# Performance work log

Measured on AMD Instinct MI355X. Metric: run time of the kernel, lower is better.

The kernel has to match this reference:

```python
import jax, jax.numpy as jnp
import numpy as np

BH, S, D = 16, 2048, 128
TEMPERATURE = float(np.sqrt(D))


def setup_inputs() -> dict:
    key = jax.random.key(0)
    kq, kk, kv = jax.random.split(key, 3)
    q = jax.random.normal(kq, (BH, S, D), dtype=jnp.float32)
    k = jax.random.normal(kk, (BH, S, D), dtype=jnp.float32)
    v = jax.random.normal(kv, (BH, S, D), dtype=jnp.float32)
    # causal mask: True = masked (filled with -inf), broadcast to every batch*head
    causal = ~jnp.tril(jnp.ones((S, S), dtype=bool))
    mask = jnp.broadcast_to(causal, (BH, S, S))
    return {"q": q, "k": k, "v": v, "mask": mask}


def reference(q, k, v, mask):
    # attn = q @ k^T / temperature, masked_fill, softmax over keys, attn @ v
    attn = jnp.einsum("bqd,bkd->bqk", q, k) / TEMPERATURE  # [BH, S, S]
    attn = jnp.where(mask, -jnp.inf, attn)
    attn = jax.nn.softmax(attn, axis=2)
    # dropout is identity in eval mode
    output = jnp.einsum("bqk,bkd->bqd", attn, v)  # [BH, S, D]
    return (output, attn)
```

## Files before the change

kernel.cpp:

```cpp
#include <hip/hip_runtime.h>
#include <hip/hip_bf16.h>

#define BH_N 16
#define SEQ 2048
#define DH 128
#define PSTR 2056

typedef __attribute__((ext_vector_type(8))) short bf16x8;
typedef __attribute__((ext_vector_type(4))) float f32x4;

__device__ __forceinline__ short f2bf(float x) {
    union { __hip_bfloat16 b; short s; } u;
    u.b = __float2bfloat16(x);
    return u.s;
}
__device__ __forceinline__ float bf2f(short s) {
    union { unsigned int u; float f; } v;
    v.u = ((unsigned int)(unsigned short)s) << 16;
    return v.f;
}

__global__ __launch_bounds__(256) void prep_kv(
    const float* __restrict__ kp, const float* __restrict__ vp,
    unsigned short* __restrict__ Kb, unsigned short* __restrict__ Vt)
{
    const int tid  = threadIdx.x;
    const int kb64 = blockIdx.x * 64;
    const int bh   = blockIdx.y;
    const float* Ksrc = kp + ((size_t)bh * SEQ + kb64) * DH;
    const float* Vsrc = vp + ((size_t)bh * SEQ + kb64) * DH;
    unsigned short* Kdst = Kb + ((size_t)bh * SEQ + kb64) * DH;
    unsigned short* Vdst = Vt + (size_t)bh * DH * SEQ + kb64;

    #pragma unroll
    for (int i = 0; i < 8; ++i) {
        const int f4 = i * 256 + tid;
        const float4 kv = *(const float4*)(Ksrc + (size_t)f4 * 4);
        ushort4 o;
        o.x = (unsigned short)f2bf(kv.x); o.y = (unsigned short)f2bf(kv.y);
        o.z = (unsigned short)f2bf(kv.z); o.w = (unsigned short)f2bf(kv.w);
        *(ushort4*)(Kdst + (size_t)f4 * 4) = o;
    }
    const int key   = tid & 63;
    const int dbase = (tid >> 6) * 4;
    #pragma unroll
    for (int j = 0; j < 8; ++j) {
        const int d0 = dbase + j * 16;
        const float4 vv = *(const float4*)(Vsrc + (size_t)key * DH + d0);
        Vdst[(size_t)(d0 + 0) * SEQ + key] = (unsigned short)f2bf(vv.x);
        Vdst[(size_t)(d0 + 1) * SEQ + key] = (unsigned short)f2bf(vv.y);
        Vdst[(size_t)(d0 + 2) * SEQ + key] = (unsigned short)f2bf(vv.z);
        Vdst[(size_t)(d0 + 3) * SEQ + key] = (unsigned short)f2bf(vv.w);
    }
}

#define LOADK4(K0, K1, K2, K3, KEYBASE) do {                                   \
    const unsigned short* kr_ = Kbh + (size_t)((KEYBASE) + c16) * DH + g * 8;  \
    K0 = *(const bf16x8*)(kr_);                                                \
    K1 = *(const bf16x8*)(kr_ + 32);                                           \
    K2 = *(const bf16x8*)(kr_ + 64);                                           \
    K3 = *(const bf16x8*)(kr_ + 96);                                           \
} while (0)

#define SW1(K0, K1, K2, K3, KEYBASE) do {                                      \
    f32x4 acc_ = {0.f, 0.f, 0.f, 0.f};                                         \
    acc_ = __builtin_amdgcn_mfma_f32_16x16x32_bf16(qf[0], K0, acc_, 0, 0, 0);  \
    acc_ = __builtin_amdgcn_mfma_f32_16x16x32_bf16(qf[1], K1, acc_, 0, 0, 0);  \
    acc_ = __builtin_amdgcn_mfma_f32_16x16x32_bf16(qf[2], K2, acc_, 0, 0, 0);  \
    acc_ = __builtin_amdgcn_mfma_f32_16x16x32_bf16(qf[3], K3, acc_, 0, 0, 0);  \
    const int key_ = (KEYBASE) + c16;                                          \
    const int qr_  = qw + g * 4;                                               \
    const float p0_ = (key_ <= qr_ + 0) ? __expf(acc_[0]) : 0.f;               \
    const float p1_ = (key_ <= qr_ + 1) ? __expf(acc_[1]) : 0.f;               \
    const float p2_ = (key_ <= qr_ + 2) ? __expf(acc_[2]) : 0.f;               \
    const float p3_ = (key_ <= qr_ + 3) ? __expf(acc_[3]) : 0.f;               \
    lsr[0] += p0_; lsr[1] += p1_; lsr[2] += p2_; lsr[3] += p3_;                \
    unsigned short* pq_ = &strip[g * 4][0] + key_;                             \
    pq_[0]        = (unsigned short)f2bf(p0_);                                 \
    pq_[PSTR]     = (unsigned short)f2bf(p1_);                                 \
    pq_[2 * PSTR] = (unsigned short)f2bf(p2_);                                 \
    pq_[3 * PSTR] = (unsigned short)f2bf(p3_);                                 \
} while (0)

#define LOADV8(V0,V1,V2,V3,V4,V5,V6,V7, KEYOFF) do {                           \
    const unsigned short* vb_ = Vbh + (size_t)c16 * SEQ + (KEYOFF) + g * 8;    \
    V0 = *(const bf16x8*)(vb_);                                                \
    V1 = *(const bf16x8*)(vb_ + 16 * SEQ);                                     \
    V2 = *(const bf16x8*)(vb_ + 32 * SEQ);                                     \
    V3 = *(const bf16x8*)(vb_ + 48 * SEQ);                                     \
    V4 = *(const bf16x8*)(vb_ + 64 * SEQ);                                     \
    V5 = *(const bf16x8*)(vb_ + 80 * SEQ);                                     \
    V6 = *(const bf16x8*)(vb_ + 96 * SEQ);                                     \
    V7 = *(const bf16x8*)(vb_ + 112 * SEQ);                                    \
} while (0)

#define PV8(PA, V0,V1,V2,V3,V4,V5,V6,V7) do {                                  \
    oacc[0] = __builtin_amdgcn_mfma_f32_16x16x32_bf16(PA, V0, oacc[0], 0, 0, 0); \
    oacc[1] = __builtin_amdgcn_mfma_f32_16x16x32_bf16(PA, V1, oacc[1], 0, 0, 0); \
    oacc[2] = __builtin_amdgcn_mfma_f32_16x16x32_bf16(PA, V2, oacc[2], 0, 0, 0); \
    oacc[3] = __builtin_amdgcn_mfma_f32_16x16x32_bf16(PA, V3, oacc[3], 0, 0, 0); \
    oacc[4] = __builtin_amdgcn_mfma_f32_16x16x32_bf16(PA, V4, oacc[4], 0, 0, 0); \
    oacc[5] = __builtin_amdgcn_mfma_f32_16x16x32_bf16(PA, V5, oacc[5], 0, 0, 0); \
    oacc[6] = __builtin_amdgcn_mfma_f32_16x16x32_bf16(PA, V6, oacc[6], 0, 0, 0); \
    oacc[7] = __builtin_amdgcn_mfma_f32_16x16x32_bf16(PA, V7, oacc[7], 0, 0, 0); \
} while (0)

__global__ __launch_bounds__(512, 4) void attn_main(
    const float* __restrict__ qp, const unsigned short* __restrict__ Kb,
    const unsigned short* __restrict__ Vt, float* __restrict__ outO,
    float* __restrict__ outA)
{
    __shared__ float lspart[8][16];
    __shared__ float lrec[16];
    __shared__ float Osh[16][132];
    __shared__ __align__(16) unsigned short strip[16][PSTR];

    const int b   = blockIdx.x;
    const int j   = b & 7;
    const int idx = b >> 3;
    const int bh  = 2 * j + (idx & 1);
    const int qt  = 127 - (idx >> 1);
    const int qw  = qt * 16;
    const size_t qbase = (size_t)bh * SEQ + qw;

    const int tid  = threadIdx.x;
    const int wv   = tid >> 6;
    const int lane = tid & 63;
    const int c16  = lane & 15;
    const int g    = lane >> 4;
    const float invT = 0.08838834764831845f;

    const unsigned short* Kbh = Kb + (size_t)bh * SEQ * DH;
    const unsigned short* Vbh = Vt + (size_t)bh * DH * SEQ;

    bf16x8 qf[4];
    {
        const float* qrow = qp + (qbase + c16) * DH + g * 8;
        #pragma unroll
        for (int c = 0; c < 4; ++c) {
            const float4 a = *(const float4*)(qrow + c * 32);
            const float4 bq = *(const float4*)(qrow + c * 32 + 4);
            bf16x8 f;
            f[0] = f2bf(a.x * invT);  f[1] = f2bf(a.y * invT);
            f[2] = f2bf(a.z * invT);  f[3] = f2bf(a.w * invT);
            f[4] = f2bf(bq.x * invT); f[5] = f2bf(bq.y * invT);
            f[6] = f2bf(bq.z * invT); f[7] = f2bf(bq.w * invT);
            qf[c] = f;
        }
    }

    float lsr[4] = {0.f, 0.f, 0.f, 0.f};
    const int n16 = qt + 1;
    {
        bf16x8 ka0, ka1, ka2, ka3, kb0, kb1, kb2, kb3;
        int t = wv;
        if (t < n16) LOADK4(ka0, ka1, ka2, ka3, t << 4);
        for (; t + 8 < n16; t += 16) {
            LOADK4(kb0, kb1, kb2, kb3, (t + 8) << 4);
            SW1(ka0, ka1, ka2, ka3, t << 4);
            if (t + 16 < n16) LOADK4(ka0, ka1, ka2, ka3, (t + 16) << 4);
            SW1(kb0, kb1, kb2, kb3, (t + 8) << 4);
        }
        if (t < n16) SW1(ka0, ka1, ka2, ka3, t << 4);
    }
    #pragma unroll
    for (int r = 0; r < 4; ++r) {
        float s = lsr[r];
        #pragma unroll
        for (int m = 1; m < 16; m <<= 1) s += __shfl_xor(s, m);
        lsr[r] = s;
    }
    if (c16 == 0) {
        #pragma unroll
        for (int r = 0; r < 4; ++r) lspart[wv][g * 4 + r] = lsr[r];
    }
    __syncthreads();
    float li[4];
    #pragma unroll
    for (int r = 0; r < 4; ++r) {
        float s = 0.f;
        #pragma unroll
        for (int w = 0; w < 8; ++w) s += lspart[w][g * 4 + r];
        li[r] = 1.f / s;
    }
    const int ns = (qw + 79) >> 6;
    if (wv == 0 && c16 == 0) {
        #pragma unroll
        for (int r = 0; r < 4; ++r) lrec[g * 4 + r] = li[r];
    }
    {
        const int row = tid >> 5;
        for (int c = n16 * 16 + (tid & 31); c < ns * 64; c += 32) strip[row][c] = 0;
    }
    __syncthreads();

    f32x4 oacc[8];
    #pragma unroll
    for (int d = 0; d < 8; ++d) oacc[d] = (f32x4){0.f, 0.f, 0.f, 0.f};

    {
        const int sr = lane >> 4;
        const int sc = (lane & 15) * 4;
        float l4[4];
        #pragma unroll
        for (int i = 0; i < 4; ++i) l4[i] = lrec[i * 4 + sr];

        bf16x8 va0, va1, va2, va3, va4, va5, va6, va7;
        bf16x8 vb0, vb1, vb2, vb3, vb4, vb5, vb6, vb7;
        for (int S = wv; S < ns; S += 8) {
            const int KB = S << 6;
            LOADV8(va0,va1,va2,va3,va4,va5,va6,va7, KB);
            LOADV8(vb0,vb1,vb2,vb3,vb4,vb5,vb6,vb7, KB + 32);
            #pragma unroll
            for (int i = 0; i < 4; ++i) {
                const int pr = i * 4 + sr;
                const unsigned short* src = &strip[pr][KB + sc];
                float4 w;
                w.x = bf2f(src[0]) * l4[i]; w.y = bf2f(src[1]) * l4[i];
                w.z = bf2f(src[2]) * l4[i]; w.w = bf2f(src[3]) * l4[i];
                *(float4*)(outA + (qbase + pr) * SEQ + KB + sc) = w;
            }
            {
                const bf16x8 pa = *(const bf16x8*)(&strip[c16][KB + g * 8]);
                PV8(pa, va0,va1,va2,va3,va4,va5,va6,va7);
            }
            {
                const bf16x8 pa = *(const bf16x8*)(&strip[c16][KB + 32 + g * 8]);
                PV8(pa, vb0,vb1,vb2,vb3,vb4,vb5,vb6,vb7);
            }
        }
    }

    for (int wp = 0; wp < 8; ++wp) {
        if (wv == wp) {
            #pragma unroll
            for (int dt = 0; dt < 8; ++dt) {
                #pragma unroll
                for (int r = 0; r < 4; ++r) {
                    const float val = oacc[dt][r] * li[r];
                    if (wp == 0) Osh[g * 4 + r][dt * 16 + c16]  = val;
                    else         Osh[g * 4 + r][dt * 16 + c16] += val;
                }
            }
        }
        __syncthreads();
    }
    {
        const int r  = tid >> 5;
        const int d0 = (tid & 31) * 4;
        float4 o;
        o.x = Osh[r][d0 + 0]; o.y = Osh[r][d0 + 1];
        o.z = Osh[r][d0 + 2]; o.w = Osh[r][d0 + 3];
        *(float4*)(outO + (qbase + r) * DH + d0) = o;
    }

    {
        const int r = tid >> 5;
        float* zrow = outA + (qbase + r) * SEQ;
        const float4 z = {0.f, 0.f, 0.f, 0.f};
        for (int c = ns * 64 + (tid & 31) * 4; c < SEQ; c += 128) {
            *(float4*)(zrow + c) = z;
        }
    }
}

__global__ __launch_bounds__(256) void attn_fallback(
    const float* __restrict__ qp, const float* __restrict__ kp,
    const float* __restrict__ vp, float* __restrict__ outO,
    float* __restrict__ outA)
{
    const int qt   = blockIdx.x;
    const int bh   = blockIdx.y;
    const int wv   = threadIdx.x >> 6;
    const int lane = threadIdx.x & 63;
    const int c16  = lane & 15;
    const int g    = lane >> 4;
    const int qw = qt * 64 + wv * 16;
    const size_t qbase = (size_t)bh * SEQ + qw;
    const float invT = 0.08838834764831845f;

    bf16x8 qf[4];
    {
        const float* qrow = qp + (qbase + c16) * DH + g * 8;
        #pragma unroll
        for (int c = 0; c < 4; ++c) {
            const float4 a = *(const float4*)(qrow + c * 32);
            const float4 bq = *(const float4*)(qrow + c * 32 + 4);
            bf16x8 f;
            f[0] = f2bf(a.x * invT);  f[1] = f2bf(a.y * invT);
            f[2] = f2bf(a.z * invT);  f[3] = f2bf(a.w * invT);
            f[4] = f2bf(bq.x * invT); f[5] = f2bf(bq.y * invT);
            f[6] = f2bf(bq.z * invT); f[7] = f2bf(bq.w * invT);
            qf[c] = f;
        }
    }
    const float* kbase = kp + (size_t)bh * SEQ * DH;
    const float* vbase = vp + (size_t)bh * SEQ * DH;

    float ls0 = 0.f, ls1 = 0.f, ls2 = 0.f, ls3 = 0.f;
    const int nkt16 = (qw + 16) >> 4;
    for (int t = 0; t < nkt16; ++t) {
        const int kb = t << 4;
        const float* krow = kbase + (size_t)(kb + c16) * DH + g * 8;
        f32x4 acc = {0.f, 0.f, 0.f, 0.f};
        #pragma unroll
        for (int c = 0; c < 4; ++c) {
            const float4 a = *(const float4*)(krow + c * 32);
            const float4 bq = *(const float4*)(krow + c * 32 + 4);
            bf16x8 f;
            f[0] = f2bf(a.x);  f[1] = f2bf(a.y);  f[2] = f2bf(a.z);  f[3] = f2bf(a.w);
            f[4] = f2bf(bq.x); f[5] = f2bf(bq.y); f[6] = f2bf(bq.z); f[7] = f2bf(bq.w);
            acc = __builtin_amdgcn_mfma_f32_16x16x32_bf16(qf[c], f, acc, 0, 0, 0);
        }
        const int key = kb + c16;
        const int qr  = qw + g * 4;
        if (key <= qr + 0) ls0 += __expf(acc[0]);
        if (key <= qr + 1) ls1 += __expf(acc[1]);
        if (key <= qr + 2) ls2 += __expf(acc[2]);
        if (key <= qr + 3) ls3 += __expf(acc[3]);
    }
    #pragma unroll
    for (int m = 1; m < 16; m <<= 1) {
        ls0 += __shfl_xor(ls0, m);
        ls1 += __shfl_xor(ls1, m);
        ls2 += __shfl_xor(ls2, m);
        ls3 += __shfl_xor(ls3, m);
    }
    const float li0 = 1.f / ls0, li1 = 1.f / ls1, li2 = 1.f / ls2, li3 = 1.f / ls3;

    __shared__ __align__(16) short ptileF[4][16][32];
    f32x4 oacc[8];
    #pragma unroll
    for (int d = 0; d < 8; ++d) oacc[d] = (f32x4){0.f, 0.f, 0.f, 0.f};

    const int n32 = (qw + 47) >> 5;
    for (int t = 0; t < n32; ++t) {
        const int kb32 = t << 5;
        #pragma unroll
        for (int h = 0; h < 2; ++h) {
            const int kb = kb32 + h * 16;
            const float* krow = kbase + (size_t)(kb + c16) * DH + g * 8;
            f32x4 acc = {0.f, 0.f, 0.f, 0.f};
            #pragma unroll
            for (int c = 0; c < 4; ++c) {
                const float4 a = *(const float4*)(krow + c * 32);
                const float4 bq = *(const float4*)(krow + c * 32 + 4);
                bf16x8 f;
                f[0] = f2bf(a.x);  f[1] = f2bf(a.y);  f[2] = f2bf(a.z);  f[3] = f2bf(a.w);
                f[4] = f2bf(bq.x); f[5] = f2bf(bq.y); f[6] = f2bf(bq.z); f[7] = f2bf(bq.w);
                acc = __builtin_amdgcn_mfma_f32_16x16x32_bf16(qf[c], f, acc, 0, 0, 0);
            }
            const int key = kb + c16;
            const int qr  = qw + g * 4;
            const float p0 = (key <= qr + 0) ? __expf(acc[0]) * li0 : 0.f;
            const float p1 = (key <= qr + 1) ? __expf(acc[1]) * li1 : 0.f;
            const float p2 = (key <= qr + 2) ? __expf(acc[2]) * li2 : 0.f;
            const float p3 = (key <= qr + 3) ? __expf(acc[3]) * li3 : 0.f;
            outA[(qbase + g * 4 + 0) * SEQ + kb + c16] = p0;
            outA[(qbase + g * 4 + 1) * SEQ + kb + c16] = p1;
            outA[(qbase + g * 4 + 2) * SEQ + kb + c16] = p2;
            outA[(qbase + g * 4 + 3) * SEQ + kb + c16] = p3;
            ptileF[wv][g * 4 + 0][h * 16 + c16] = f2bf(p0);
            ptileF[wv][g * 4 + 1][h * 16 + c16] = f2bf(p1);
            ptileF[wv][g * 4 + 2][h * 16 + c16] = f2bf(p2);
            ptileF[wv][g * 4 + 3][h * 16 + c16] = f2bf(p3);
        }
        bf16x8 pa = *(bf16x8*)&ptileF[wv][c16][g * 8];
        #pragma unroll
        for (int dt = 0; dt < 8; ++dt) {
            const float* vcol = vbase + (size_t)(kb32 + g * 8) * DH + dt * 16 + c16;
            bf16x8 vf;
            #pragma unroll
            for (int i = 0; i < 8; ++i) vf[i] = f2bf(vcol[(size_t)i * DH]);
            oacc[dt] = __builtin_amdgcn_mfma_f32_16x16x32_bf16(pa, vf, oacc[dt], 0, 0, 0);
        }
    }
    {
        const float4 z4 = {0.f, 0.f, 0.f, 0.f};
        float* zrow = outA + (qbase + (lane >> 2)) * SEQ;
        for (int c = n32 * 32 + (lane & 3) * 8; c < SEQ; c += 32) {
            *(float4*)(zrow + c)     = z4;
            *(float4*)(zrow + c + 4) = z4;
        }
    }
    #pragma unroll
    for (int dt = 0; dt < 8; ++dt) {
        #pragma unroll
        for (int r = 0; r < 4; ++r) {
            outO[(qbase + g * 4 + r) * DH + dt * 16 + c16] = oacc[dt][r];
        }
    }
}

extern "C" void kernel_launch(void* const* d_in, const int* in_sizes, int n_in,
                              void* d_out, int out_size, void* d_ws, size_t ws_size,
                              hipStream_t stream) {
    (void)in_sizes; (void)n_in; (void)out_size;
    const float* q = (const float*)d_in[0];
    const float* k = (const float*)d_in[1];
    const float* v = (const float*)d_in[2];
    float* outO = (float*)d_out;
    float* outA = outO + (size_t)BH_N * SEQ * DH;

    const size_t need = (size_t)BH_N * SEQ * DH * sizeof(unsigned short) * 2;
    if (ws_size >= need) {
        unsigned short* Kb = (unsigned short*)d_ws;
        unsigned short* Vt = Kb + (size_t)BH_N * SEQ * DH;
        prep_kv<<<dim3(SEQ / 64, BH_N), 256, 0, stream>>>(k, v, Kb, Vt);
        attn_main<<<dim3(2048), 512, 0, stream>>>(q, Kb, Vt, outO, outA);
    } else {
        attn_fallback<<<dim3(SEQ / 64, BH_N), 256, 0, stream>>>(q, k, v, outO, outA);
    }
}
```

Measured before the change: 176.0 us.

## Deepen K/V prefetch pipelines and replace serialized O reduction with parallel slab sum

The K-tile phase now keeps four tiles of K loads in flight per wave instead of two. The PV loop now prefetches the next V tiles while the MFMAs for the current tile run. The cross-wave O reduction drops its loop of eight barriers: each wave writes a private slab into shared memory that aliases the probability strip, and all threads then sum the slabs in parallel. The cost is more registers and a larger aliased shared buffer, which may lower occupancy. A strange no-op line was also added to the fallback kernel.

```diff
diff --git a/kernel.cpp b/kernel.cpp
--- a/kernel.cpp
+++ b/kernel.cpp
@@ -14,9 +14,9 @@
     u.b = __float2bfloat16(x);
     return u.s;
 }
-__device__ __forceinline__ float bf2f(short s) {
+__device__ __forceinline__ float bf2f(unsigned short s) {
     union { unsigned int u; float f; } v;
-    v.u = ((unsigned int)(unsigned short)s) << 16;
+    v.u = ((unsigned int)s) << 16;
     return v.f;
 }
 
@@ -112,8 +112,9 @@
 {
     __shared__ float lspart[8][16];
     __shared__ float lrec[16];
-    __shared__ float Osh[16][132];
-    __shared__ __align__(16) unsigned short strip[16][PSTR];
+    __shared__ __align__(16) unsigned char smem[8 * 2116 * 4];
+    unsigned short (*strip)[PSTR] = (unsigned short(*)[PSTR])smem;
+    float* Oall = (float*)smem;
 
     const int b   = blockIdx.x;
     const int j   = b & 7;
@@ -152,16 +153,22 @@
     float lsr[4] = {0.f, 0.f, 0.f, 0.f};
     const int n16 = qt + 1;
     {
-        bf16x8 ka0, ka1, ka2, ka3, kb0, kb1, kb2, kb3;
+        bf16x8 k00,k01,k02,k03, k10,k11,k12,k13, k20,k21,k22,k23, k30,k31,k32,k33;
         int t = wv;
-        if (t < n16) LOADK4(ka0, ka1, ka2, ka3, t << 4);
-        for (; t + 8 < n16; t += 16) {
-            LOADK4(kb0, kb1, kb2, kb3, (t + 8) << 4);
-            SW1(ka0, ka1, ka2, ka3, t << 4);
-            if (t + 16 < n16) LOADK4(ka0, ka1, ka2, ka3, (t + 16) << 4);
-            SW1(kb0, kb1, kb2, kb3, (t + 8) << 4);
-        }
-        if (t < n16) SW1(ka0, ka1, ka2, ka3, t << 4);
+        if (t < n16)      LOADK4(k00,k01,k02,k03, t << 4);
+        if (t + 8 < n16)  LOADK4(k10,k11,k12,k13, (t + 8) << 4);
+        if (t + 16 < n16) LOADK4(k20,k21,k22,k23, (t + 16) << 4);
+        if (t + 24 < n16) LOADK4(k30,k31,k32,k33, (t + 24) << 4);
+        for (; t + 32 < n16; t += 32) {
+            SW1(k00,k01,k02,k03, t << 4);        LOADK4(k00,k01,k02,k03, (t + 32) << 4);
+            SW1(k10,k11,k12,k13, (t + 8) << 4);  LOADK4(k10,k11,k12,k13, (t + 40) << 4);
+            SW1(k20,k21,k22,k23, (t + 16) << 4); LOADK4(k20,k21,k22,k23, (t + 48) << 4);
+            SW1(k30,k31,k32,k33, (t + 24) << 4); LOADK4(k30,k31,k32,k33, (t + 56) << 4);
+        }
+        if (t < n16)      SW1(k00,k01,k02,k03, t << 4);
+        if (t + 8 < n16)  SW1(k10,k11,k12,k13, (t + 8) << 4);
+        if (t + 16 < n16) SW1(k20,k21,k22,k23, (t + 16) << 4);
+        if (t + 24 < n16) SW1(k30,k31,k32,k33, (t + 24) << 4);
     }
     #pragma unroll
     for (int r = 0; r < 4; ++r) {
@@ -205,12 +212,15 @@
         #pragma unroll
         for (int i = 0; i < 4; ++i) l4[i] = lrec[i * 4 + sr];
 
-        bf16x8 va0, va1, va2, va3, va4, va5, va6, va7;
-        bf16x8 vb0, vb1, vb2, vb3, vb4, vb5, vb6, vb7;
-        for (int S = wv; S < ns; S += 8) {
+        bf16x8 va0,va1,va2,va3,va4,va5,va6,va7;
+        bf16x8 vb0,vb1,vb2,vb3,vb4,vb5,vb6,vb7;
+        int S = wv;
+        if (S < ns) {
+            LOADV8(va0,va1,va2,va3,va4,va5,va6,va7, S << 6);
+            LOADV8(vb0,vb1,vb2,vb3,vb4,vb5,vb6,vb7, (S << 6) + 32);
+        }
+        for (; S < ns; S += 8) {
             const int KB = S << 6;
-            LOADV8(va0,va1,va2,va3,va4,va5,va6,va7, KB);
-            LOADV8(vb0,vb1,vb2,vb3,vb4,vb5,vb6,vb7, KB + 32);
             #pragma unroll
             for (int i = 0; i < 4; ++i) {
                 const int pr = i * 4 + sr;
@@ -224,34 +234,38 @@
                 const bf16x8 pa = *(const bf16x8*)(&strip[c16][KB + g * 8]);
                 PV8(pa, va0,va1,va2,va3,va4,va5,va6,va7);
             }
+            if (S + 8 < ns) LOADV8(va0,va1,va2,va3,va4,va5,va6,va7, (S + 8) << 6);
             {
                 const bf16x8 pa = *(const bf16x8*)(&strip[c16][KB + 32 + g * 8]);
                 PV8(pa, vb0,vb1,vb2,vb3,vb4,vb5,vb6,vb7);
             }
-        }
-    }
-
-    for (int wp = 0; wp < 8; ++wp) {
-        if (wv == wp) {
+            if (S + 8 < ns) LOADV8(vb0,vb1,vb2,vb3,vb4,vb5,vb6,vb7, ((S + 8) << 6) + 32);
+        }
+    }
+
+    __syncthreads();
+    {
+        float* slab = Oall + wv * 2116;
+        #pragma unroll
+        for (int dt = 0; dt < 8; ++dt) {
             #pragma unroll
-            for (int dt = 0; dt < 8; ++dt) {
-                #pragma unroll
-                for (int r = 0; r < 4; ++r) {
-                    const float val = oacc[dt][r] * li[r];
-                    if (wp == 0) Osh[g * 4 + r][dt * 16 + c16]  = val;
-                    else         Osh[g * 4 + r][dt * 16 + c16] += val;
-                }
+            for (int r = 0; r < 4; ++r) {
+                slab[(g * 4 + r) * 132 + dt * 16 + c16] = oacc[dt][r] * li[r];
             }
         }
-        __syncthreads();
-    }
-    {
-        const int r  = tid >> 5;
-        const int d0 = (tid & 31) * 4;
-        float4 o;
-        o.x = Osh[r][d0 + 0]; o.y = Osh[r][d0 + 1];
-        o.z = Osh[r][d0 + 2]; o.w = Osh[r][d0 + 3];
-        *(float4*)(outO + (qbase + r) * DH + d0) = o;
+    }
+    __syncthreads();
+    {
+        const int row = tid >> 5;
+        const int d0  = (tid & 31) * 4;
+        float sx = 0.f, sy = 0.f, sz = 0.f, sw = 0.f;
+        #pragma unroll
+        for (int w = 0; w < 8; ++w) {
+            const float* p = Oall + w * 2116 + row * 132 + d0;
+            sx += p[0]; sy += p[1]; sz += p[2]; sw += p[3];
+        }
+        float4 o; o.x = sx; o.y = sy; o.z = sz; o.w = sw;
+        *(float4*)(outO + (qbase + row) * DH + d0) = o;
     }
 
     {
@@ -371,6 +385,8 @@
             const float* vcol = vbase + (size_t)(kb32 + g * 8) * DH + dt * 16 + c16;
             bf16x8 vf;
             #pragma unroll
+            for (int i = 0; i < 8; ++i) vf[i] = f2bf((unsigned short)f2bf(vcol[(size_t)i * DH]) ) , vf[i] = f2bf(vcol[(size_t)i * DH]) ? 0 : 0;
+            #pragma unroll
             for (int i = 0; i < 8; ++i) vf[i] = f2bf(vcol[(size_t)i * DH]);
             oacc[dt] = __builtin_amdgcn_mfma_f32_16x16x32_bf16(pa, vf, oacc[dt], 0, 0, 0);
         }
```

Result: slower. 190.3 us (+8.1%).

## Split attention into P-sweep and PV/store kernels via global bf16 P buffer

Applied to the files above, without the earlier changes.

Splits the fused attention kernel into two launches. The first computes exp(QK^T) tiles into a global bf16 P workspace plus reciprocal row sums. The second reads P back to write the normalized attention matrix and compute P@V. This removes the large per-block LDS strip (16x2056 bf16) so more blocks can be resident, but adds a global round trip of up to 128 MB of P traffic, an extra launch, and a larger workspace requirement. If the workspace is too small, it falls back to the slow path.

```diff
diff --git a/kernel.cpp b/kernel.cpp
--- a/kernel.cpp
+++ b/kernel.cpp
@@ -4,19 +4,19 @@
 #define BH_N 16
 #define SEQ 2048
 #define DH 128
-#define PSTR 2056
 
 typedef __attribute__((ext_vector_type(8))) short bf16x8;
 typedef __attribute__((ext_vector_type(4))) float f32x4;
+typedef __attribute__((ext_vector_type(4))) int int4v;
 
 __device__ __forceinline__ short f2bf(float x) {
     union { __hip_bfloat16 b; short s; } u;
     u.b = __float2bfloat16(x);
     return u.s;
 }
-__device__ __forceinline__ float bf2f(short s) {
+__device__ __forceinline__ float bf2f(unsigned short s) {
     union { unsigned int u; float f; } v;
-    v.u = ((unsigned int)(unsigned short)s) << 16;
+    v.u = ((unsigned int)s) << 16;
     return v.f;
 }
 
@@ -62,7 +62,7 @@
     K3 = *(const bf16x8*)(kr_ + 96);                                           \
 } while (0)
 
-#define SW1(K0, K1, K2, K3, KEYBASE) do {                                      \
+#define QKH2(K0, K1, K2, K3, KEYBASE, HH) do {                                 \
     f32x4 acc_ = {0.f, 0.f, 0.f, 0.f};                                         \
     acc_ = __builtin_amdgcn_mfma_f32_16x16x32_bf16(qf[0], K0, acc_, 0, 0, 0);  \
     acc_ = __builtin_amdgcn_mfma_f32_16x16x32_bf16(qf[1], K1, acc_, 0, 0, 0);  \
@@ -75,12 +75,98 @@
     const float p2_ = (key_ <= qr_ + 2) ? __expf(acc_[2]) : 0.f;               \
     const float p3_ = (key_ <= qr_ + 3) ? __expf(acc_[3]) : 0.f;               \
     lsr[0] += p0_; lsr[1] += p1_; lsr[2] += p2_; lsr[3] += p3_;                \
-    unsigned short* pq_ = &strip[g * 4][0] + key_;                             \
-    pq_[0]        = (unsigned short)f2bf(p0_);                                 \
-    pq_[PSTR]     = (unsigned short)f2bf(p1_);                                 \
-    pq_[2 * PSTR] = (unsigned short)f2bf(p2_);                                 \
-    pq_[3 * PSTR] = (unsigned short)f2bf(p3_);                                 \
+    const int cc_ = (HH) * 16 + c16;                                           \
+    ptile[wv][g * 4 + 0][cc_] = (unsigned short)f2bf(p0_);                     \
+    ptile[wv][g * 4 + 1][cc_] = (unsigned short)f2bf(p1_);                     \
+    ptile[wv][g * 4 + 2][cc_] = (unsigned short)f2bf(p2_);                     \
+    ptile[wv][g * 4 + 3][cc_] = (unsigned short)f2bf(p3_);                     \
 } while (0)
+
+#define PTB(T) ((((size_t)(bh * 128 + qt)) * 64 + (T)) * 512)
+
+__global__ __launch_bounds__(512, 4) void p_sweep(
+    const float* __restrict__ qp, const unsigned short* __restrict__ Kb,
+    unsigned short* __restrict__ Pp, float* __restrict__ Li)
+{
+    __shared__ float lspart[8][16];
+    __shared__ __align__(16) unsigned short ptile[8][16][40];
+
+    const int b   = blockIdx.x;
+    const int j   = b & 7;
+    const int idx = b >> 3;
+    const int bh  = 2 * j + (idx & 1);
+    const int qt  = 127 - (idx >> 1);
+    const int qw  = qt * 16;
+    const size_t qbase = (size_t)bh * SEQ + qw;
+
+    const int tid  = threadIdx.x;
+    const int wv   = tid >> 6;
+    const int lane = tid & 63;
+    const int c16  = lane & 15;
+    const int g    = lane >> 4;
+    const float invT = 0.08838834764831845f;
+
+    const unsigned short* Kbh = Kb + (size_t)bh * SEQ * DH;
+
+    bf16x8 qf[4];
+    {
+        const float* qrow = qp + (qbase + c16) * DH + g * 8;
+        #pragma unroll
+        for (int c = 0; c < 4; ++c) {
+            const float4 a = *(const float4*)(qrow + c * 32);
+            const float4 bq = *(const float4*)(qrow + c * 32 + 4);
+            bf16x8 f;
+            f[0] = f2bf(a.x * invT);  f[1] = f2bf(a.y * invT);
+            f[2] = f2bf(a.z * invT);  f[3] = f2bf(a.w * invT);
+            f[4] = f2bf(bq.x * invT); f[5] = f2bf(bq.y * invT);
+            f[6] = f2bf(bq.z * invT); f[7] = f2bf(bq.w * invT);
+            qf[c] = f;
+        }
+    }
+
+    float lsr[4] = {0.f, 0.f, 0.f, 0.f};
+    const int n32 = (qw + 47) >> 5;
+    {
+        const int prow = lane >> 2;
+        const int pcol = (lane & 3) * 8;
+        bf16x8 ka0, ka1, ka2, ka3, kb0, kb1, kb2, kb3;
+        int t = wv;
+        if (t < n32) LOADK4(ka0, ka1, ka2, ka3, t << 5);
+        for (; t < n32; t += 8) {
+            const int kb32 = t << 5;
+            LOADK4(kb0, kb1, kb2, kb3, kb32 + 16);
+            QKH2(ka0, ka1, ka2, ka3, kb32, 0);
+            if (t + 8 < n32) LOADK4(ka0, ka1, ka2, ka3, (t + 8) << 5);
+            QKH2(kb0, kb1, kb2, kb3, kb32 + 16, 1);
+            *(int4v*)(Pp + PTB(t) + prow * 32 + pcol) = *(int4v*)&ptile[wv][prow][pcol];
+        }
+    }
+    {
+        const int ns = (qw + 79) >> 6;
+        const int gap = 2 * ns - n32;
+        for (int i = tid; i < gap * 512; i += 512) {
+            Pp[PTB(n32) + i] = 0;
+        }
+    }
+    #pragma unroll
+    for (int r = 0; r < 4; ++r) {
+        float s = lsr[r];
+        #pragma unroll
+        for (int m = 1; m < 16; m <<= 1) s += __shfl_xor(s, m);
+        lsr[r] = s;
+    }
+    if (c16 == 0) {
+        #pragma unroll
+        for (int r = 0; r < 4; ++r) lspart[wv][g * 4 + r] = lsr[r];
+    }
+    __syncthreads();
+    if (tid < 16) {
+        float s = 0.f;
+        #pragma unroll
+        for (int w = 0; w < 8; ++w) s += lspart[w][tid];
+        Li[qbase + tid] = 1.f / s;
+    }
+}
 
 #define LOADV8(V0,V1,V2,V3,V4,V5,V6,V7, KEYOFF) do {                           \
     const unsigned short* vb_ = Vbh + (size_t)c16 * SEQ + (KEYOFF) + g * 8;    \
@@ -105,15 +191,13 @@
     oacc[7] = __builtin_amdgcn_mfma_f32_16x16x32_bf16(PA, V7, oacc[7], 0, 0, 0); \
 } while (0)
 
-__global__ __launch_bounds__(512, 4) void attn_main(
-    const float* __restrict__ qp, const unsigned short* __restrict__ Kb,
+__global__ __launch_bounds__(512, 4) void pv_store(
+    const unsigned short* __restrict__ Pp, const float* __restrict__ Li,
     const unsigned short* __restrict__ Vt, float* __restrict__ outO,
     float* __restrict__ outA)
 {
-    __shared__ float lspart[8][16];
     __shared__ float lrec[16];
     __shared__ float Osh[16][132];
-    __shared__ __align__(16) unsigned short strip[16][PSTR];
 
     const int b   = blockIdx.x;
     const int j   = b & 7;
@@ -128,82 +212,29 @@
     const int lane = tid & 63;
     const int c16  = lane & 15;
     const int g    = lane >> 4;
-    const float invT = 0.08838834764831845f;
-
-    const unsigned short* Kbh = Kb + (size_t)bh * SEQ * DH;
+
     const unsigned short* Vbh = Vt + (size_t)bh * DH * SEQ;
 
-    bf16x8 qf[4];
-    {
-        const float* qrow = qp + (qbase + c16) * DH + g * 8;
-        #pragma unroll
-        for (int c = 0; c < 4; ++c) {
-            const float4 a = *(const float4*)(qrow + c * 32);
-            const float4 bq = *(const float4*)(qrow + c * 32 + 4);
-            bf16x8 f;
-            f[0] = f2bf(a.x * invT);  f[1] = f2bf(a.y * invT);
-            f[2] = f2bf(a.z * invT);  f[3] = f2bf(a.w * invT);
-            f[4] = f2bf(bq.x * invT); f[5] = f2bf(bq.y * invT);
-            f[6] = f2bf(bq.z * invT); f[7] = f2bf(bq.w * invT);
-            qf[c] = f;
-        }
-    }
-
-    float lsr[4] = {0.f, 0.f, 0.f, 0.f};
-    const int n16 = qt + 1;
-    {
-        bf16x8 ka0, ka1, ka2, ka3, kb0, kb1, kb2, kb3;
-        int t = wv;
-        if (t < n16) LOADK4(ka0, ka1, ka2, ka3, t << 4);
-        for (; t + 8 < n16; t += 16) {
-            LOADK4(kb0, kb1, kb2, kb3, (t + 8) << 4);
-            SW1(ka0, ka1, ka2, ka3, t << 4);
-            if (t + 16 < n16) LOADK4(ka0, ka1, ka2, ka3, (t + 16) << 4);
-            SW1(kb0, kb1, kb2, kb3, (t + 8) << 4);
-        }
-        if (t < n16) SW1(ka0, ka1, ka2, ka3, t << 4);
-    }
-    #pragma unroll
-    for (int r = 0; r < 4; ++r) {
-        float s = lsr[r];
-        #pragma unroll
-        for (int m = 1; m < 16; m <<= 1) s += __shfl_xor(s, m);
-        lsr[r] = s;
-    }
-    if (c16 == 0) {
-        #pragma unroll
-        for (int r = 0; r < 4; ++r) lspart[wv][g * 4 + r] = lsr[r];
-    }
+    if (tid < 16) lrec[tid] = Li[qbase + tid];
     __syncthreads();
+
     float li[4];
     #pragma unroll
-    for (int r = 0; r < 4; ++r) {
-        float s = 0.f;
-        #pragma unroll
-        for (int w = 0; w < 8; ++w) s += lspart[w][g * 4 + r];
-        li[r] = 1.f / s;
-    }
+    for (int r = 0; r < 4; ++r) li[r] = lrec[g * 4 + r];
+
+    f32x4 oacc[8];
+    #pragma unroll
+    for (int d = 0; d < 8; ++d) oacc[d] = (f32x4){0.f, 0.f, 0.f, 0.f};
+
     const int ns = (qw + 79) >> 6;
-    if (wv == 0 && c16 == 0) {
-        #pragma unroll
-        for (int r = 0; r < 4; ++r) lrec[g * 4 + r] = li[r];
-    }
-    {
-        const int row = tid >> 5;
-        for (int c = n16 * 16 + (tid & 31); c < ns * 64; c += 32) strip[row][c] = 0;
-    }
-    __syncthreads();
-
-    f32x4 oacc[8];
-    #pragma unroll
-    for (int d = 0; d < 8; ++d) oacc[d] = (f32x4){0.f, 0.f, 0.f, 0.f};
-
     {
         const int sr = lane >> 4;
         const int sc = (lane & 15) * 4;
         float l4[4];
         #pragma unroll
         for (int i = 0; i < 4; ++i) l4[i] = lrec[i * 4 + sr];
+        const int st_t  = sc >> 5;
+        const int st_ki = sc & 31;
 
         bf16x8 va0, va1, va2, va3, va4, va5, va6, va7;
         bf16x8 vb0, vb1, vb2, vb3, vb4, vb5, vb6, vb7;
@@ -214,18 +245,18 @@
             #pragma unroll
             for (int i = 0; i < 4; ++i) {
                 const int pr = i * 4 + sr;
-                const unsigned short* src = &strip[pr][KB + sc];
+                const ushort4 p4 = *(const ushort4*)(Pp + PTB(2 * S + st_t) + pr * 32 + st_ki);
                 float4 w;
-                w.x = bf2f(src[0]) * l4[i]; w.y = bf2f(src[1]) * l4[i];
-                w.z = bf2f(src[2]) * l4[i]; w.w = bf2f(src[3]) * l4[i];
+                w.x = bf2f(p4.x) * l4[i]; w.y = bf2f(p4.y) * l4[i];
+                w.z = bf2f(p4.z) * l4[i]; w.w = bf2f(p4.w) * l4[i];
                 *(float4*)(outA + (qbase + pr) * SEQ + KB + sc) = w;
             }
             {
-                const bf16x8 pa = *(const bf16x8*)(&strip[c16][KB + g * 8]);
+                const bf16x8 pa = *(const bf16x8*)(Pp + PTB(2 * S) + c16 * 32 + g * 8);
                 PV8(pa, va0,va1,va2,va3,va4,va5,va6,va7);
             }
             {
-                const bf16x8 pa = *(const bf16x8*)(&strip[c16][KB + 32 + g * 8]);
+                const bf16x8 pa = *(const bf16x8*)(Pp + PTB(2 * S + 1) + c16 * 32 + g * 8);
                 PV8(pa, vb0,vb1,vb2,vb3,vb4,vb5,vb6,vb7);
             }
         }
@@ -402,12 +433,19 @@
     float* outO = (float*)d_out;
     float* outA = outO + (size_t)BH_N * SEQ * DH;
 
-    const size_t need = (size_t)BH_N * SEQ * DH * sizeof(unsigned short) * 2;
+    const size_t kvb   = (size_t)BH_N * SEQ * DH;
+    const size_t ppb   = (size_t)BH_N * SEQ * SEQ;
+    const size_t lib   = (size_t)BH_N * SEQ;
+    const size_t need  = (2 * kvb + ppb) * sizeof(unsigned short) + lib * sizeof(float);
+
     if (ws_size >= need) {
         unsigned short* Kb = (unsigned short*)d_ws;
-        unsigned short* Vt = Kb + (size_t)BH_N * SEQ * DH;
+        unsigned short* Vt = Kb + kvb;
+        unsigned short* Pp = Vt + kvb;
+        float*          Li = (float*)(Pp + ppb);
         prep_kv<<<dim3(SEQ / 64, BH_N), 256, 0, stream>>>(k, v, Kb, Vt);
-        attn_main<<<dim3(2048), 512, 0, stream>>>(q, Kb, Vt, outO, outA);
+        p_sweep<<<dim3(2048), 512, 0, stream>>>(q, Kb, Pp, Li);
+        pv_store<<<dim3(2048), 512, 0, stream>>>(Pp, Li, Vt, outO, outA);
     } else {
         attn_fallback<<<dim3(SEQ / 64, BH_N), 256, 0, stream>>>(q, k, v, outO, outA);
     }
```

Result: slower. 202.0 us (+14.8%).
